# Optimization experiments

Measured on AMD Instinct MI355X. Metric: run time of the kernel, lower is better.

## Reference

```python
import jax, jax.numpy as jnp
import numpy as np

HEADS = 8
DIM_HEAD = 64
SCALE = DIM_HEAD ** -0.5


def setup_inputs() -> dict:
    key = jax.random.key(0)
    k1, k2, k3, k4 = jax.random.split(key, 4)
    b, n, dim = 2, 2048, 512
    inner = HEADS * DIM_HEAD  # 512
    x = jax.random.normal(k1, (b, n, dim), dtype=jnp.float32)
    adj = jax.random.uniform(k2, (b, n, n), dtype=jnp.float32)
    w_qkv = jax.random.normal(k3, (dim, 3 * inner), dtype=jnp.float32) * (dim ** -0.5)
    w_out = jax.random.normal(k4, (inner, dim), dtype=jnp.float32) * (inner ** -0.5)
    b_out = jnp.zeros((dim,), dtype=jnp.float32)
    return {"x": x, "adj": adj, "w_qkv": w_qkv, "w_out": w_out, "b_out": b_out}


def reference(x, adj, w_qkv, w_out, b_out):
    b, n, dim = x.shape
    qkv = x @ w_qkv  # [b, n, 3*inner]
    q, k, v = jnp.split(qkv, 3, axis=-1)
    # [b, n, h*d] -> [b, h, n, d]
    reshape = lambda t: t.reshape(b, n, HEADS, DIM_HEAD).transpose(0, 2, 1, 3)
    q, k, v = reshape(q), reshape(k), reshape(v)
    dots = jnp.einsum('bhid,bhjd->bhij', q, k) * SCALE  # [b, h, n, n]
    # softmax over adjacency rows, broadcast across heads, multiply into scores
    mask = jax.nn.softmax(adj, axis=-1)[:, None, :, :]  # [b, 1, n, n]
    attn = jax.nn.softmax(mask * dots, axis=-1)
    out = jnp.einsum('bhij,bhjd->bhid', attn, v)  # [b, h, n, d]
    out = out.transpose(0, 2, 1, 3).reshape(b, n, HEADS * DIM_HEAD)
    return out @ w_out + b_out
```

## Files before the change

### kernel.cpp

```cpp
#include <hip/hip_runtime.h>
#include <hip/hip_bf16.h>
#include <math.h>

#define BB 2
#define NN 2048
#define DIM 512
#define NH 8
#define HD 64
#define SCALE 0.125f

typedef __bf16 bf16x8 __attribute__((ext_vector_type(8)));
typedef __bf16 bf16x4 __attribute__((ext_vector_type(4)));
typedef float floatx4 __attribute__((ext_vector_type(4)));

static inline __device__ floatx4 mfma16(bf16x8 a, bf16x8 b, floatx4 c) {
    return __builtin_amdgcn_mfma_f32_16x16x32_bf16(a, b, c, 0, 0, 0);
}

static inline __device__ bf16x8 cvt8(float4 a, float4 b) {
    bf16x8 r;
    r[0] = (__bf16)a.x; r[1] = (__bf16)a.y; r[2] = (__bf16)a.z; r[3] = (__bf16)a.w;
    r[4] = (__bf16)b.x; r[5] = (__bf16)b.y; r[6] = (__bf16)b.z; r[7] = (__bf16)b.w;
    return r;
}

static inline __device__ float bf2f(unsigned short u) {
    return __uint_as_float(((unsigned)u) << 16);
}

__global__ __launch_bounds__(256) void adj_softmax(const float* __restrict__ adj,
                                                   __bf16* __restrict__ mask) {
    int row = blockIdx.x;
    const float* a = adj + (size_t)row * NN;
    __bf16* m = mask + (size_t)row * NN;
    int t = threadIdx.x;
    float v[8];
    float mx = -INFINITY;
#pragma unroll
    for (int c = 0; c < 8; ++c) { v[c] = a[t + 256 * c]; mx = fmaxf(mx, v[c]); }
    __shared__ float red[256];
    red[t] = mx; __syncthreads();
    for (int s = 128; s > 0; s >>= 1) {
        if (t < s) red[t] = fmaxf(red[t], red[t + s]);
        __syncthreads();
    }
    mx = red[0]; __syncthreads();
    float sm = 0.f;
    float e[8];
#pragma unroll
    for (int c = 0; c < 8; ++c) { e[c] = __expf(v[c] - mx); sm += e[c]; }
    red[t] = sm; __syncthreads();
    for (int s = 128; s > 0; s >>= 1) {
        if (t < s) red[t] += red[t + s];
        __syncthreads();
    }
    float inv = 1.0f / red[0];
#pragma unroll
    for (int c = 0; c < 8; ++c) m[t + 256 * c] = (__bf16)(e[c] * inv);
}

__global__ __launch_bounds__(256) void tcast_w(const float* __restrict__ w,
                                               __bf16* __restrict__ wT,
                                               int K, int N) {
    __shared__ float tile[32][33];
    int n0 = blockIdx.x * 32, k0 = blockIdx.y * 32;
    int c = threadIdx.x & 31, r = threadIdx.x >> 5;
#pragma unroll
    for (int p = 0; p < 4; ++p)
        tile[r + p * 8][c] = w[(size_t)(k0 + r + p * 8) * N + n0 + c];
    __syncthreads();
#pragma unroll
    for (int p = 0; p < 4; ++p)
        wT[(size_t)(n0 + r + p * 8) * K + k0 + c] = (__bf16)tile[c][r + p * 8];
}

__global__ __launch_bounds__(256) void qkv_mfma(const float* __restrict__ x,
                                                const __bf16* __restrict__ wT,
                                                __bf16* __restrict__ q,
                                                __bf16* __restrict__ kk,
                                                __bf16* __restrict__ vT) {
    __shared__ __bf16 As[128 * 40];
    __shared__ __bf16 Bs[128 * 40];
    const int t = threadIdx.x;
    const int lane = t & 63, w = t >> 6;
    const int n16 = lane & 15, quad = lane >> 4;
    const int wm = w >> 1, wn = w & 1;
    const int m0 = blockIdx.y * 128, n0 = blockIdx.x * 128;
    const int r1 = t >> 2, seg = t & 3;

    floatx4 acc[4][4];
#pragma unroll
    for (int mt = 0; mt < 4; ++mt)
#pragma unroll
        for (int nt = 0; nt < 4; ++nt) acc[mt][nt] = (floatx4){0.f, 0.f, 0.f, 0.f};

    for (int k0 = 0; k0 < 512; k0 += 32) {
        const float* xs1 = x + (size_t)(m0 + r1) * 512 + k0 + seg * 8;
        const float* xs2 = xs1 + (size_t)64 * 512;
        float4 fa1 = *(const float4*)xs1, fa2 = *(const float4*)(xs1 + 4);
        float4 fb1 = *(const float4*)xs2, fb2 = *(const float4*)(xs2 + 4);
        bf16x8 a1 = cvt8(fa1, fa2), a2 = cvt8(fb1, fb2);
        bf16x8 w1 = *(const bf16x8*)(wT + (size_t)(n0 + r1) * 512 + k0 + seg * 8);
        bf16x8 w2 = *(const bf16x8*)(wT + (size_t)(n0 + r1 + 64) * 512 + k0 + seg * 8);
        __syncthreads();
        *(bf16x8*)(As + r1 * 40 + seg * 8) = a1;
        *(bf16x8*)(As + (r1 + 64) * 40 + seg * 8) = a2;
        *(bf16x8*)(Bs + r1 * 40 + seg * 8) = w1;
        *(bf16x8*)(Bs + (r1 + 64) * 40 + seg * 8) = w2;
        __syncthreads();
        bf16x8 af[4], bf[4];
#pragma unroll
        for (int mt = 0; mt < 4; ++mt)
            af[mt] = *(const bf16x8*)(As + (wm * 64 + mt * 16 + n16) * 40 + quad * 8);
#pragma unroll
        for (int nt = 0; nt < 4; ++nt)
            bf[nt] = *(const bf16x8*)(Bs + (wn * 64 + nt * 16 + n16) * 40 + quad * 8);
#pragma unroll
        for (int mt = 0; mt < 4; ++mt)
#pragma unroll
            for (int nt = 0; nt < 4; ++nt)
                acc[mt][nt] = mfma16(af[mt], bf[nt], acc[mt][nt]);
    }

#pragma unroll
    for (int mt = 0; mt < 4; ++mt)
#pragma unroll
        for (int nt = 0; nt < 4; ++nt)
#pragma unroll
            for (int r = 0; r < 4; ++r) {
                int m = m0 + wm * 64 + mt * 16 + quad * 4 + r;
                int n = n0 + wn * 64 + nt * 16 + n16;
                int b = m >> 11, i = m & 2047;
                int sg = n >> 9, cc = n & 511;
                int h = cc >> 6, d = cc & 63;
                size_t bh = (size_t)(b * NH + h);
                float fv = acc[mt][nt][r];
                if (sg == 0)      q[(bh * NN + i) * HD + d] = (__bf16)(fv * SCALE);
                else if (sg == 1) kk[(bh * NN + i) * HD + d] = (__bf16)fv;
                else              vT[(bh * HD + d) * NN + i] = (__bf16)fv;
            }
}

__global__ __launch_bounds__(256, 4) void flash_attn(const __bf16* __restrict__ qb,
                                                     const __bf16* __restrict__ kb,
                                                     const __bf16* __restrict__ vTb,
                                                     const __bf16* __restrict__ maskb,
                                                     __bf16* __restrict__ Opart,
                                                     float* __restrict__ lpart) {
    __shared__ __bf16 Ks[64][72];
    __shared__ __bf16 Vs[64][72];
    __shared__ __bf16 Ps[64][72];
    __shared__ float Lrow[64];

    const int t = threadIdx.x;
    const int lane = t & 63;
    const int w = t >> 6;
    const int n16 = lane & 15;
    const int quad = lane >> 4;

    const int blk = blockIdx.x;
    const int split = blk & 1;
    const int it = (blk >> 1) & 31;
    const int h = (blk >> 6) & 7;
    const int b = blk >> 9;
    const int i0 = it * 64;
    const int bh = b * NH + h;

    bf16x8 qfrag[2];
    {
        const __bf16* qrow = qb + ((size_t)bh * NN + i0 + w * 16 + n16) * HD;
        qfrag[0] = *(const bf16x8*)(qrow + quad * 8);
        qfrag[1] = *(const bf16x8*)(qrow + 32 + quad * 8);
    }

    floatx4 O[4];
#pragma unroll
    for (int dt = 0; dt < 4; ++dt) O[dt] = (floatx4){0.f, 0.f, 0.f, 0.f};
    float lp = 0.f;

    const int srow = t >> 3, sseg = t & 7;
    const __bf16* kg = kb + (size_t)bh * NN * HD;
    const __bf16* vg = vTb + (size_t)bh * HD * NN;
    const __bf16* mbase = maskb + ((size_t)b * NN + i0 + w * 16 + n16) * NN;

    int j0 = split * (NN / 2);
    float4 k1 = *(const float4*)(kg + (size_t)(j0 + srow) * HD + sseg * 8);
    float4 k2 = *(const float4*)(kg + (size_t)(j0 + srow + 32) * HD + sseg * 8);
    float4 v1 = *(const float4*)(vg + (size_t)srow * NN + j0 + sseg * 8);
    float4 v2 = *(const float4*)(vg + (size_t)(srow + 32) * NN + j0 + sseg * 8);

    for (int iter = 0; iter < (NN / 2) / 64; ++iter, j0 += 64) {
        __syncthreads();
        *(float4*)(&Ks[srow][sseg * 8]) = k1;
        *(float4*)(&Ks[srow + 32][sseg * 8]) = k2;
        *(float4*)(&Vs[srow][sseg * 8]) = v1;
        *(float4*)(&Vs[srow + 32][sseg * 8]) = v2;
        __syncthreads();
        if (iter + 1 < (NN / 2) / 64) {
            int jn = j0 + 64;
            k1 = *(const float4*)(kg + (size_t)(jn + srow) * HD + sseg * 8);
            k2 = *(const float4*)(kg + (size_t)(jn + srow + 32) * HD + sseg * 8);
            v1 = *(const float4*)(vg + (size_t)srow * NN + jn + sseg * 8);
            v2 = *(const float4*)(vg + (size_t)(srow + 32) * NN + jn + sseg * 8);
        }
        ushort4 mu[4];
        const __bf16* mrow = mbase + j0 + quad * 4;
#pragma unroll
        for (int jt = 0; jt < 4; ++jt)
            mu[jt] = *(const ushort4*)(mrow + jt * 16);

        floatx4 S[4];
#pragma unroll
        for (int jt = 0; jt < 4; ++jt) {
            floatx4 acc = (floatx4){0.f, 0.f, 0.f, 0.f};
            bf16x8 kf0 = *(const bf16x8*)(&Ks[jt * 16 + n16][quad * 8]);
            bf16x8 kf1 = *(const bf16x8*)(&Ks[jt * 16 + n16][32 + quad * 8]);
            acc = mfma16(kf0, qfrag[0], acc);
            acc = mfma16(kf1, qfrag[1], acc);
            S[jt] = acc;
        }

#pragma unroll
        for (int jt = 0; jt < 4; ++jt) {
            float p0 = __expf(S[jt][0] * bf2f(mu[jt].x));
            float p1 = __expf(S[jt][1] * bf2f(mu[jt].y));
            float p2 = __expf(S[jt][2] * bf2f(mu[jt].z));
            float p3 = __expf(S[jt][3] * bf2f(mu[jt].w));
            lp += (p0 + p1) + (p2 + p3);
            bf16x4 pk;
            pk[0] = (__bf16)p0; pk[1] = (__bf16)p1;
            pk[2] = (__bf16)p2; pk[3] = (__bf16)p3;
            *(bf16x4*)(&Ps[w * 16 + n16][jt * 16 + quad * 4]) = pk;
        }

        bf16x8 pf0 = *(const bf16x8*)(&Ps[w * 16 + n16][quad * 8]);
        bf16x8 pf1 = *(const bf16x8*)(&Ps[w * 16 + n16][32 + quad * 8]);
#pragma unroll
        for (int dt = 0; dt < 4; ++dt) {
            bf16x8 vf0 = *(const bf16x8*)(&Vs[dt * 16 + n16][quad * 8]);
            bf16x8 vf1 = *(const bf16x8*)(&Vs[dt * 16 + n16][32 + quad * 8]);
            O[dt] = mfma16(pf0, vf0, O[dt]);
            O[dt] = mfma16(pf1, vf1, O[dt]);
        }
    }

    lp += __shfl_xor(lp, 16);
    lp += __shfl_xor(lp, 32);
    const size_t sb = (size_t)(split * BB * NH + bh);
    if (quad == 0) {
        Lrow[w * 16 + n16] = lp;
        lpart[sb * NN + i0 + w * 16 + n16] = lp;
    }
#pragma unroll
    for (int dt = 0; dt < 4; ++dt)
#pragma unroll
        for (int r = 0; r < 4; ++r) {
            int i = i0 + w * 16 + quad * 4 + r;
            int d = dt * 16 + n16;
            Opart[(sb * NN + i) * HD + d] = (__bf16)O[dt][r];
        }
}

__global__ __launch_bounds__(256) void combine(const __bf16* __restrict__ Opart,
                                               const float* __restrict__ lpart,
                                               __bf16* __restrict__ ohb) {
    int g = blockIdx.x * 256 + threadIdx.x;
    int d0 = (g & 7) * 8;
    int n = (g >> 3) & 2047;
    int bh = g >> 14;
    int b = bh >> 3, h = bh & 7;
    size_t idx0 = ((size_t)bh * NN + n) * HD + d0;
    size_t idx1 = ((size_t)(BB * NH + bh) * NN + n) * HD + d0;
    bf16x8 o0 = *(const bf16x8*)(Opart + idx0);
    bf16x8 o1 = *(const bf16x8*)(Opart + idx1);
    float l = lpart[(size_t)bh * NN + n] + lpart[(size_t)(BB * NH + bh) * NN + n];
    float inv = 1.0f / l;
    bf16x8 r;
#pragma unroll
    for (int e = 0; e < 8; ++e)
        r[e] = (__bf16)(((float)o0[e] + (float)o1[e]) * inv);
    *(bf16x8*)(ohb + ((size_t)b * NN + n) * (NH * HD) + h * HD + d0) = r;
}

__global__ __launch_bounds__(256) void out_mfma(const __bf16* __restrict__ A,
                                                const __bf16* __restrict__ wT,
                                                const float* __restrict__ bias,
                                                float* __restrict__ out) {
    __shared__ __bf16 As[64 * 40];
    __shared__ __bf16 Bs[128 * 40];
    const int t = threadIdx.x;
    const int lane = t & 63, w = t >> 6;
    const int n16 = lane & 15, quad = lane >> 4;
    const int wm = w >> 1, wn = w & 1;
    const int m0 = blockIdx.y * 64, n0 = blockIdx.x * 128;
    const int ra = t >> 2, seg = t & 3;
    const int rb = t >> 2;

    floatx4 acc[2][4];
#pragma unroll
    for (int mt = 0; mt < 2; ++mt)
#pragma unroll
        for (int nt = 0; nt < 4; ++nt) acc[mt][nt] = (floatx4){0.f, 0.f, 0.f, 0.f};

    for (int k0 = 0; k0 < 512; k0 += 32) {
        bf16x8 a1 = *(const bf16x8*)(A + (size_t)(m0 + ra) * 512 + k0 + seg * 8);
        bf16x8 w1 = *(const bf16x8*)(wT + (size_t)(n0 + rb) * 512 + k0 + seg * 8);
        bf16x8 w2 = *(const bf16x8*)(wT + (size_t)(n0 + rb + 64) * 512 + k0 + seg * 8);
        __syncthreads();
        *(bf16x8*)(As + ra * 40 + seg * 8) = a1;
        *(bf16x8*)(Bs + rb * 40 + seg * 8) = w1;
        *(bf16x8*)(Bs + (rb + 64) * 40 + seg * 8) = w2;
        __syncthreads();
        bf16x8 af[2], bf[4];
#pragma unroll
        for (int mt = 0; mt < 2; ++mt)
            af[mt] = *(const bf16x8*)(As + (wm * 32 + mt * 16 + n16) * 40 + quad * 8);
#pragma unroll
        for (int nt = 0; nt < 4; ++nt)
            bf[nt] = *(const bf16x8*)(Bs + (wn * 64 + nt * 16 + n16) * 40 + quad * 8);
#pragma unroll
        for (int mt = 0; mt < 2; ++mt)
#pragma unroll
            for (int nt = 0; nt < 4; ++nt)
                acc[mt][nt] = mfma16(af[mt], bf[nt], acc[mt][nt]);
    }

#pragma unroll
    for (int mt = 0; mt < 2; ++mt)
#pragma unroll
        for (int nt = 0; nt < 4; ++nt)
#pragma unroll
            for (int r = 0; r < 4; ++r) {
                int m = m0 + wm * 32 + mt * 16 + quad * 4 + r;
                int n = n0 + wn * 64 + nt * 16 + n16;
                out[(size_t)m * 512 + n] = acc[mt][nt][r] + bias[n];
            }
}

extern "C" void kernel_launch(void* const* d_in, const int* in_sizes, int n_in,
                              void* d_out, int out_size, void* d_ws, size_t ws_size,
                              hipStream_t stream) {
    const float* x     = (const float*)d_in[0];
    const float* adj   = (const float*)d_in[1];
    const float* w_qkv = (const float*)d_in[2];
    const float* w_out = (const float*)d_in[3];
    const float* b_out = (const float*)d_in[4];
    float* out = (float*)d_out;
    char* wsb = (char*)d_ws;

    __bf16* wqkvT = (__bf16*)(wsb + 0);
    __bf16* woutT = (__bf16*)(wsb + (3u << 19));
    __bf16* q     = (__bf16*)(wsb + (2u << 20));
    __bf16* ohb   = (__bf16*)(wsb + (2u << 20));
    __bf16* k     = (__bf16*)(wsb + (6u << 20));
    __bf16* vT    = (__bf16*)(wsb + (10u << 20));
    __bf16* mask  = (__bf16*)(wsb + (14u << 20));
    __bf16* Opart = (__bf16*)(wsb + (30u << 20));
    float*  lpart = (float*) (wsb + (46u << 20));

    adj_softmax<<<BB * NN, 256, 0, stream>>>(adj, mask);
    tcast_w<<<dim3(1536 / 32, 512 / 32), 256, 0, stream>>>(w_qkv, wqkvT, 512, 1536);
    tcast_w<<<dim3(512 / 32, 512 / 32), 256, 0, stream>>>(w_out, woutT, 512, 512);
    qkv_mfma<<<dim3(1536 / 128, 4096 / 128), 256, 0, stream>>>(x, wqkvT, q, k, vT);
    flash_attn<<<BB * NH * 32 * 2, 256, 0, stream>>>(q, k, vT, mask, Opart, lpart);
    combine<<<1024, 256, 0, stream>>>(Opart, lpart, ohb);
    out_mfma<<<dim3(512 / 128, 4096 / 64), 256, 0, stream>>>(ohb, woutT, b_out, out);
}
```

Baseline: 181.8 us.

## Use direct global-to-LDS loads in GEMMs, pre-cast x, and split attention four ways

The fp32 input x is now cast to bf16 in a separate kernel. The QKV and output-projection GEMMs then load their tiles straight from global memory into LDS with `global_load_lds`, using an XOR-swizzled layout in place of the padded one. The QKV tile shrinks to 128x64, and flash attention splits the key range four ways instead of two, with `combine` summing four partials. The adjacency softmax also switches to vectorized float4 loads and bf16x4 stores. The aim is to cut register staging and LDS bank conflicts and to raise parallelism, at the cost of an extra kernel launch and more partial-output traffic.

```diff
diff --git a/kernel.cpp b/kernel.cpp
--- a/kernel.cpp
+++ b/kernel.cpp
@@ -28,16 +28,25 @@
     return __uint_as_float(((unsigned)u) << 16);
 }
 
+static inline __device__ void dma16(const void* g, void* l) {
+    __builtin_amdgcn_global_load_lds(
+        (const __attribute__((address_space(1))) unsigned int*)g,
+        (__attribute__((address_space(3))) unsigned int*)l,
+        16, 0, 0);
+}
+
 __global__ __launch_bounds__(256) void adj_softmax(const float* __restrict__ adj,
                                                    __bf16* __restrict__ mask) {
     int row = blockIdx.x;
     const float* a = adj + (size_t)row * NN;
     __bf16* m = mask + (size_t)row * NN;
     int t = threadIdx.x;
-    float v[8];
+    float4 va = *(const float4*)(a + 4 * t);
+    float4 vb = *(const float4*)(a + 1024 + 4 * t);
+    float v[8] = {va.x, va.y, va.z, va.w, vb.x, vb.y, vb.z, vb.w};
     float mx = -INFINITY;
 #pragma unroll
-    for (int c = 0; c < 8; ++c) { v[c] = a[t + 256 * c]; mx = fmaxf(mx, v[c]); }
+    for (int c = 0; c < 8; ++c) mx = fmaxf(mx, v[c]);
     __shared__ float red[256];
     red[t] = mx; __syncthreads();
     for (int s = 128; s > 0; s >>= 1) {
@@ -55,8 +64,19 @@
         __syncthreads();
     }
     float inv = 1.0f / red[0];
-#pragma unroll
-    for (int c = 0; c < 8; ++c) m[t + 256 * c] = (__bf16)(e[c] * inv);
+    bf16x4 o0, o1;
+#pragma unroll
+    for (int c = 0; c < 4; ++c) { o0[c] = (__bf16)(e[c] * inv); o1[c] = (__bf16)(e[c + 4] * inv); }
+    *(bf16x4*)(m + 4 * t) = o0;
+    *(bf16x4*)(m + 1024 + 4 * t) = o1;
+}
+
+__global__ __launch_bounds__(256) void xcast(const float* __restrict__ x,
+                                             __bf16* __restrict__ xb) {
+    int g = blockIdx.x * 256 + threadIdx.x;
+    float4 f0 = ((const float4*)x)[2 * (size_t)g];
+    float4 f1 = ((const float4*)x)[2 * (size_t)g + 1];
+    *(bf16x8*)(xb + 8 * (size_t)g) = cvt8(f0, f1);
 }
 
 __global__ __launch_bounds__(256) void tcast_w(const float* __restrict__ w,
@@ -74,62 +94,60 @@
         wT[(size_t)(n0 + r + p * 8) * K + k0 + c] = (__bf16)tile[c][r + p * 8];
 }
 
-__global__ __launch_bounds__(256) void qkv_mfma(const float* __restrict__ x,
+__global__ __launch_bounds__(256) void qkv_mfma(const __bf16* __restrict__ xb,
                                                 const __bf16* __restrict__ wT,
                                                 __bf16* __restrict__ q,
                                                 __bf16* __restrict__ kk,
                                                 __bf16* __restrict__ vT) {
-    __shared__ __bf16 As[128 * 40];
-    __shared__ __bf16 Bs[128 * 40];
+    __shared__ __bf16 As[128 * 32];
+    __shared__ __bf16 Bs[64 * 32];
     const int t = threadIdx.x;
     const int lane = t & 63, w = t >> 6;
     const int n16 = lane & 15, quad = lane >> 4;
     const int wm = w >> 1, wn = w & 1;
-    const int m0 = blockIdx.y * 128, n0 = blockIdx.x * 128;
-    const int r1 = t >> 2, seg = t & 3;
-
-    floatx4 acc[4][4];
+    const int m0 = blockIdx.y * 128, n0 = blockIdx.x * 64;
+
+    const int drow = t >> 2;
+    const int dchunk = (t & 3) ^ (drow & 3);
+    char* ldsA = (char*)As + (t >> 6) * 1024;
+    char* ldsB = (char*)Bs + (t >> 6) * 1024;
+
+    floatx4 acc[4][2];
 #pragma unroll
     for (int mt = 0; mt < 4; ++mt)
 #pragma unroll
-        for (int nt = 0; nt < 4; ++nt) acc[mt][nt] = (floatx4){0.f, 0.f, 0.f, 0.f};
+        for (int nt = 0; nt < 2; ++nt) acc[mt][nt] = (floatx4){0.f, 0.f, 0.f, 0.f};
+
+    const int swz = n16 & 3;
 
     for (int k0 = 0; k0 < 512; k0 += 32) {
-        const float* xs1 = x + (size_t)(m0 + r1) * 512 + k0 + seg * 8;
-        const float* xs2 = xs1 + (size_t)64 * 512;
-        float4 fa1 = *(const float4*)xs1, fa2 = *(const float4*)(xs1 + 4);
-        float4 fb1 = *(const float4*)xs2, fb2 = *(const float4*)(xs2 + 4);
-        bf16x8 a1 = cvt8(fa1, fa2), a2 = cvt8(fb1, fb2);
-        bf16x8 w1 = *(const bf16x8*)(wT + (size_t)(n0 + r1) * 512 + k0 + seg * 8);
-        bf16x8 w2 = *(const bf16x8*)(wT + (size_t)(n0 + r1 + 64) * 512 + k0 + seg * 8);
-        __syncthreads();
-        *(bf16x8*)(As + r1 * 40 + seg * 8) = a1;
-        *(bf16x8*)(As + (r1 + 64) * 40 + seg * 8) = a2;
-        *(bf16x8*)(Bs + r1 * 40 + seg * 8) = w1;
-        *(bf16x8*)(Bs + (r1 + 64) * 40 + seg * 8) = w2;
-        __syncthreads();
-        bf16x8 af[4], bf[4];
+        __syncthreads();
+        dma16(xb + (size_t)(m0 + drow) * 512 + k0 + dchunk * 8, ldsA);
+        dma16(xb + (size_t)(m0 + 64 + drow) * 512 + k0 + dchunk * 8, (char*)As + 4096 + (t >> 6) * 1024);
+        dma16(wT + (size_t)(n0 + drow) * 512 + k0 + dchunk * 8, ldsB);
+        __syncthreads();
+        bf16x8 af[4], bf[2];
 #pragma unroll
         for (int mt = 0; mt < 4; ++mt)
-            af[mt] = *(const bf16x8*)(As + (wm * 64 + mt * 16 + n16) * 40 + quad * 8);
-#pragma unroll
-        for (int nt = 0; nt < 4; ++nt)
-            bf[nt] = *(const bf16x8*)(Bs + (wn * 64 + nt * 16 + n16) * 40 + quad * 8);
+            af[mt] = *(const bf16x8*)(As + (wm * 64 + mt * 16 + n16) * 32 + (quad ^ swz) * 8);
+#pragma unroll
+        for (int nt = 0; nt < 2; ++nt)
+            bf[nt] = *(const bf16x8*)(Bs + (wn * 32 + nt * 16 + n16) * 32 + (quad ^ swz) * 8);
 #pragma unroll
         for (int mt = 0; mt < 4; ++mt)
 #pragma unroll
-            for (int nt = 0; nt < 4; ++nt)
+            for (int nt = 0; nt < 2; ++nt)
                 acc[mt][nt] = mfma16(af[mt], bf[nt], acc[mt][nt]);
     }
 
 #pragma unroll
     for (int mt = 0; mt < 4; ++mt)
 #pragma unroll
-        for (int nt = 0; nt < 4; ++nt)
+        for (int nt = 0; nt < 2; ++nt)
 #pragma unroll
             for (int r = 0; r < 4; ++r) {
                 int m = m0 + wm * 64 + mt * 16 + quad * 4 + r;
-                int n = n0 + wn * 64 + nt * 16 + n16;
+                int n = n0 + wn * 32 + nt * 16 + n16;
                 int b = m >> 11, i = m & 2047;
                 int sg = n >> 9, cc = n & 511;
                 int h = cc >> 6, d = cc & 63;
@@ -150,7 +168,6 @@
     __shared__ __bf16 Ks[64][72];
     __shared__ __bf16 Vs[64][72];
     __shared__ __bf16 Ps[64][72];
-    __shared__ float Lrow[64];
 
     const int t = threadIdx.x;
     const int lane = t & 63;
@@ -159,10 +176,10 @@
     const int quad = lane >> 4;
 
     const int blk = blockIdx.x;
-    const int split = blk & 1;
-    const int it = (blk >> 1) & 31;
-    const int h = (blk >> 6) & 7;
-    const int b = blk >> 9;
+    const int split = blk & 3;
+    const int it = (blk >> 2) & 31;
+    const int h = (blk >> 7) & 7;
+    const int b = blk >> 10;
     const int i0 = it * 64;
     const int bh = b * NH + h;
 
@@ -183,20 +200,20 @@
     const __bf16* vg = vTb + (size_t)bh * HD * NN;
     const __bf16* mbase = maskb + ((size_t)b * NN + i0 + w * 16 + n16) * NN;
 
-    int j0 = split * (NN / 2);
+    int j0 = split * (NN / 4);
     float4 k1 = *(const float4*)(kg + (size_t)(j0 + srow) * HD + sseg * 8);
     float4 k2 = *(const float4*)(kg + (size_t)(j0 + srow + 32) * HD + sseg * 8);
     float4 v1 = *(const float4*)(vg + (size_t)srow * NN + j0 + sseg * 8);
     float4 v2 = *(const float4*)(vg + (size_t)(srow + 32) * NN + j0 + sseg * 8);
 
-    for (int iter = 0; iter < (NN / 2) / 64; ++iter, j0 += 64) {
+    for (int iter = 0; iter < (NN / 4) / 64; ++iter, j0 += 64) {
         __syncthreads();
         *(float4*)(&Ks[srow][sseg * 8]) = k1;
         *(float4*)(&Ks[srow + 32][sseg * 8]) = k2;
         *(float4*)(&Vs[srow][sseg * 8]) = v1;
         *(float4*)(&Vs[srow + 32][sseg * 8]) = v2;
         __syncthreads();
-        if (iter + 1 < (NN / 2) / 64) {
+        if (iter + 1 < (NN / 4) / 64) {
             int jn = j0 + 64;
             k1 = *(const float4*)(kg + (size_t)(jn + srow) * HD + sseg * 8);
             k2 = *(const float4*)(kg + (size_t)(jn + srow + 32) * HD + sseg * 8);
@@ -247,10 +264,8 @@
     lp += __shfl_xor(lp, 16);
     lp += __shfl_xor(lp, 32);
     const size_t sb = (size_t)(split * BB * NH + bh);
-    if (quad == 0) {
-        Lrow[w * 16 + n16] = lp;
+    if (quad == 0)
         lpart[sb * NN + i0 + w * 16 + n16] = lp;
-    }
 #pragma unroll
     for (int dt = 0; dt < 4; ++dt)
 #pragma unroll
@@ -269,16 +284,20 @@
     int n = (g >> 3) & 2047;
     int bh = g >> 14;
     int b = bh >> 3, h = bh & 7;
-    size_t idx0 = ((size_t)bh * NN + n) * HD + d0;
-    size_t idx1 = ((size_t)(BB * NH + bh) * NN + n) * HD + d0;
-    bf16x8 o0 = *(const bf16x8*)(Opart + idx0);
-    bf16x8 o1 = *(const bf16x8*)(Opart + idx1);
-    float l = lpart[(size_t)bh * NN + n] + lpart[(size_t)(BB * NH + bh) * NN + n];
+    float o[8] = {};
+    float l = 0.f;
+#pragma unroll
+    for (int s = 0; s < 4; ++s) {
+        size_t sb = (size_t)(s * BB * NH + bh);
+        bf16x8 ov = *(const bf16x8*)(Opart + (sb * NN + n) * HD + d0);
+#pragma unroll
+        for (int e = 0; e < 8; ++e) o[e] += (float)ov[e];
+        l += lpart[sb * NN + n];
+    }
     float inv = 1.0f / l;
     bf16x8 r;
 #pragma unroll
-    for (int e = 0; e < 8; ++e)
-        r[e] = (__bf16)(((float)o0[e] + (float)o1[e]) * inv);
+    for (int e = 0; e < 8; ++e) r[e] = (__bf16)(o[e] * inv);
     *(bf16x8*)(ohb + ((size_t)b * NN + n) * (NH * HD) + h * HD + d0) = r;
 }
 
@@ -286,15 +305,19 @@
                                                 const __bf16* __restrict__ wT,
                                                 const float* __restrict__ bias,
                                                 float* __restrict__ out) {
-    __shared__ __bf16 As[64 * 40];
-    __shared__ __bf16 Bs[128 * 40];
+    __shared__ __bf16 As[64 * 32];
+    __shared__ __bf16 Bs[128 * 32];
     const int t = threadIdx.x;
     const int lane = t & 63, w = t >> 6;
     const int n16 = lane & 15, quad = lane >> 4;
     const int wm = w >> 1, wn = w & 1;
     const int m0 = blockIdx.y * 64, n0 = blockIdx.x * 128;
-    const int ra = t >> 2, seg = t & 3;
-    const int rb = t >> 2;
+
+    const int drow = t >> 2;
+    const int dchunk = (t & 3) ^ (drow & 3);
+    char* ldsA = (char*)As + (t >> 6) * 1024;
+    char* ldsB = (char*)Bs + (t >> 6) * 1024;
+    const int swz = n16 & 3;
 
     floatx4 acc[2][4];
 #pragma unroll
@@ -303,21 +326,18 @@
         for (int nt = 0; nt < 4; ++nt) acc[mt][nt] = (floatx4){0.f, 0.f, 0.f, 0.f};
 
     for (int k0 = 0; k0 < 512; k0 += 32) {
-        bf16x8 a1 = *(const bf16x8*)(A + (size_t)(m0 + ra) * 512 + k0 + seg * 8);
-        bf16x8 w1 = *(const bf16x8*)(wT + (size_t)(n0 + rb) * 512 + k0 + seg * 8);
-        bf16x8 w2 = *(const bf16x8*)(wT + (size_t)(n0 + rb + 64) * 512 + k0 + seg * 8);
-        __syncthreads();
-        *(bf16x8*)(As + ra * 40 + seg * 8) = a1;
-        *(bf16x8*)(Bs + rb * 40 + seg * 8) = w1;
-        *(bf16x8*)(Bs + (rb + 64) * 40 + seg * 8) = w2;
+        __syncthreads();
+        dma16(A + (size_t)(m0 + drow) * 512 + k0 + dchunk * 8, ldsA);
+        dma16(wT + (size_t)(n0 + drow) * 512 + k0 + dchunk * 8, ldsB);
+        dma16(wT + (size_t)(n0 + 64 + drow) * 512 + k0 + dchunk * 8, (char*)Bs + 4096 + (t >> 6) * 1024);
         __syncthreads();
         bf16x8 af[2], bf[4];
 #pragma unroll
         for (int mt = 0; mt < 2; ++mt)
-            af[mt] = *(const bf16x8*)(As + (wm * 32 + mt * 16 + n16) * 40 + quad * 8);
+            af[mt] = *(const bf16x8*)(As + (wm * 32 + mt * 16 + n16) * 32 + (quad ^ swz) * 8);
 #pragma unroll
         for (int nt = 0; nt < 4; ++nt)
-            bf[nt] = *(const bf16x8*)(Bs + (wn * 64 + nt * 16 + n16) * 40 + quad * 8);
+            bf[nt] = *(const bf16x8*)(Bs + (wn * 64 + nt * 16 + n16) * 32 + (quad ^ swz) * 8);
 #pragma unroll
         for (int mt = 0; mt < 2; ++mt)
 #pragma unroll
@@ -356,13 +376,15 @@
     __bf16* vT    = (__bf16*)(wsb + (10u << 20));
     __bf16* mask  = (__bf16*)(wsb + (14u << 20));
     __bf16* Opart = (__bf16*)(wsb + (30u << 20));
+    __bf16* xb    = (__bf16*)(wsb + (30u << 20));
     float*  lpart = (float*) (wsb + (46u << 20));
 
     adj_softmax<<<BB * NN, 256, 0, stream>>>(adj, mask);
+    xcast<<<1024, 256, 0, stream>>>(x, xb);
     tcast_w<<<dim3(1536 / 32, 512 / 32), 256, 0, stream>>>(w_qkv, wqkvT, 512, 1536);
     tcast_w<<<dim3(512 / 32, 512 / 32), 256, 0, stream>>>(w_out, woutT, 512, 512);
-    qkv_mfma<<<dim3(1536 / 128, 4096 / 128), 256, 0, stream>>>(x, wqkvT, q, k, vT);
-    flash_attn<<<BB * NH * 32 * 2, 256, 0, stream>>>(q, k, vT, mask, Opart, lpart);
+    qkv_mfma<<<dim3(1536 / 64, 4096 / 128), 256, 0, stream>>>(xb, wqkvT, q, k, vT);
+    flash_attn<<<BB * NH * 32 * 4, 256, 0, stream>>>(q, k, vT, mask, Opart, lpart);
     combine<<<1024, 256, 0, stream>>>(Opart, lpart, ohb);
     out_mfma<<<dim3(512 / 128, 4096 / 64), 256, 0, stream>>>(ohb, woutT, b_out, out);
 }
```

Result: faster. 175.7 us (-3.3%).
